# Performance work log

Hardware: AMD Instinct MI355X
Metric: run time of the kernel (lower is better)

Reference implementation:

```python
import jax, jax.numpy as jnp
import numpy as np
import math

HEADS = 16


def setup_inputs() -> dict:
    key = jax.random.key(0)
    kx, kq, kk, kv = jax.random.split(key, 4)
    B, S, E = 2, 2048, 1024
    x = jax.random.normal(kx, (B, S, E), dtype=jnp.float32)
    # torch nn.Linear weights are [out, in]; y = x @ W.T
    Wq = jax.random.normal(kq, (E, E), dtype=jnp.float32) * (1.0 / math.sqrt(E))
    Wk = jax.random.normal(kk, (E, E), dtype=jnp.float32) * (1.0 / math.sqrt(E))
    Wv = jax.random.normal(kv, (E, E), dtype=jnp.float32) * (1.0 / math.sqrt(E))
    # multiplicative causal mask, as the module applies mask by elementwise multiply
    mask = jnp.tril(jnp.ones((S, S), dtype=jnp.float32))
    return {"x": x, "Wq": Wq, "Wk": Wk, "Wv": Wv, "mask": mask}


def reference(x, Wq, Wk, Wv, mask):
    B, S, E = x.shape
    H = HEADS
    D = E // H
    q = (x @ Wq.T).reshape(B, S, H, D)
    k = (x @ Wk.T).reshape(B, S, H, D)
    v = (x @ Wv.T).reshape(B, S, H, D)
    # scores: [B, H, S, S]
    sim = jnp.einsum('nqhd,nkhd->nhqk', q, k)
    sim = sim * mask  # multiplicative mask, broadcast over (B, H)
    # NOTE: original scales by sqrt(emsize), not sqrt(head_dim)
    attn = jax.nn.softmax(sim / math.sqrt(E), axis=-1)
    out = jnp.einsum('nhql,nlhd->nqhd', attn, v).reshape(B, S, E)
    return out
```

## Files before the change

kernel.cpp:

```cpp
#include <hip/hip_runtime.h>
#include <hip/hip_bf16.h>
#include <cstdint>

using bf16   = __bf16;
using bf16x4 = __attribute__((ext_vector_type(4))) __bf16;
using bf16x8 = __attribute__((ext_vector_type(8))) __bf16;
using f32x4  = __attribute__((ext_vector_type(4))) float;

#define MFMA16(a, b, c) __builtin_amdgcn_mfma_f32_16x16x32_bf16((a), (b), (c), 0, 0, 0)

__device__ __forceinline__ void load_lds16(const bf16* g, bf16* l) {
    __builtin_amdgcn_global_load_lds(
        (const __attribute__((address_space(1))) void*)g,
        (__attribute__((address_space(3))) void*)l, 16, 0, 0);
}

__global__ __launch_bounds__(256) void cast_all(const float* __restrict__ x,
                                                const float* __restrict__ Wq,
                                                const float* __restrict__ Wk,
                                                const float* __restrict__ Wv,
                                                bf16* __restrict__ xb,
                                                bf16* __restrict__ wb,
                                                float qscale) {
    int i = blockIdx.x * 256 + threadIdx.x;
    const float* src; bf16* dst; int off; float scale = 1.0f;
    if (i < 1048576)      { src = x;  dst = xb;              off = i; }
    else if (i < 1310720) { src = Wq; dst = wb;              off = i - 1048576; scale = qscale; }
    else if (i < 1572864) { src = Wk; dst = wb + (1u << 20); off = i - 1310720; }
    else                  { src = Wv; dst = wb + (2u << 20); off = i - 1572864; }
    float4 v = reinterpret_cast<const float4*>(src)[off];
    bf16x4 o;
    o[0] = (bf16)(v.x * scale); o[1] = (bf16)(v.y * scale);
    o[2] = (bf16)(v.z * scale); o[3] = (bf16)(v.w * scale);
    reinterpret_cast<bf16x4*>(dst)[off] = o;
}

__global__ __launch_bounds__(256) void qkv_gemm(const bf16* __restrict__ xb,
                                                const bf16* __restrict__ wb,
                                                bf16* __restrict__ Qo,
                                                bf16* __restrict__ Ko,
                                                bf16* __restrict__ Vt) {
    const int n0 = blockIdx.x * 128;
    const int m0 = blockIdx.y * 128;

    __shared__ __align__(16) bf16 As[128 * 64];
    __shared__ __align__(16) bf16 Bs[128 * 64];

    const int t    = threadIdx.x;
    const int lane = t & 63;
    const int wid  = t >> 6;
    const int quad = lane >> 4;
    const int col  = lane & 15;
    const int wm   = wid & 1;
    const int wn   = wid >> 1;

    const int rsub = lane >> 3;
    const int csw  = ((lane & 7) ^ rsub) * 8;

    f32x4 acc[4][4] = {};

    const bf16* Ag = &xb[(size_t)(m0 + rsub) * 1024 + csw];
    const bf16* Bg = &wb[(size_t)(n0 + rsub) * 1024 + csw];

    for (int kc = 0; kc < 1024; kc += 64) {
        __syncthreads();
#pragma unroll
        for (int j = 0; j < 4; ++j) {
            const int c = wid * 4 + j;
            load_lds16(Ag + kc + (size_t)c * 8 * 1024, &As[c * 512]);
        }
#pragma unroll
        for (int j = 0; j < 4; ++j) {
            const int c = wid * 4 + j;
            load_lds16(Bg + kc + (size_t)c * 8 * 1024, &Bs[c * 512]);
        }
        __syncthreads();

#pragma unroll
        for (int ks = 0; ks < 2; ++ks) {
            const int ca = ((ks * 4 + quad) ^ (col & 7)) * 8;
            bf16x8 a[4], b[4];
#pragma unroll
            for (int i = 0; i < 4; ++i)
                a[i] = *reinterpret_cast<const bf16x8*>(
                    &As[(wm * 64 + i * 16 + col) * 64 + ca]);
#pragma unroll
            for (int i = 0; i < 4; ++i)
                b[i] = *reinterpret_cast<const bf16x8*>(
                    &Bs[(wn * 64 + i * 16 + col) * 64 + ca]);
#pragma unroll
            for (int mt = 0; mt < 4; ++mt)
#pragma unroll
                for (int nt = 0; nt < 4; ++nt)
                    acc[mt][nt] = MFMA16(a[mt], b[nt], acc[mt][nt]);
        }
    }

    const int w = blockIdx.x >> 3;
#pragma unroll
    for (int mt = 0; mt < 4; ++mt) {
#pragma unroll
        for (int nt = 0; nt < 4; ++nt) {
#pragma unroll
            for (int r = 0; r < 4; ++r) {
                int m = m0 + wm * 64 + mt * 16 + quad * 4 + r;
                int n = n0 + wn * 64 + nt * 16 + col;
                int bb = m >> 11, s = m & 2047;
                int n1 = n & 1023;
                int h = n1 >> 6, d = n1 & 63;
                size_t bh = (size_t)(bb * 16 + h);
                bf16 v = (bf16)acc[mt][nt][r];
                if (w == 0)      Qo[(bh * 2048 + s) * 64 + d] = v;
                else if (w == 1) Ko[(bh * 2048 + s) * 64 + d] = v;
                else             Vt[(bh * 64 + d) * 2048 + s] = v;
            }
        }
    }
}

__global__ __launch_bounds__(256) void tail_kernel(const bf16* __restrict__ Vt,
                                                   float* __restrict__ Tail) {
    const int bh = blockIdx.x;
    const bf16* Vg = Vt + (size_t)bh * 64 * 2048;
    float* Tg = Tail + (size_t)bh * 33 * 64;

    __shared__ float ts[64 * 33];
    const int tid = threadIdx.x;

#pragma unroll
    for (int i = 0; i < 8; ++i) {
        int task = i * 256 + tid;
        int d = task >> 5, tt = task & 31;
        const bf16* p = &Vg[(size_t)d * 2048 + tt * 64];
        float s = 0.0f;
#pragma unroll
        for (int j = 0; j < 8; ++j) {
            bf16x8 v = *reinterpret_cast<const bf16x8*>(p + j * 8);
#pragma unroll
            for (int e = 0; e < 8; ++e) s += (float)v[e];
        }
        ts[d * 33 + tt] = s;
    }
    __syncthreads();

    if (tid < 64) {
        const int d = tid;
        float s = 0.0f;
        Tg[32 * 64 + d] = 0.0f;
        for (int tt = 31; tt >= 1; --tt) {
            s += ts[d * 33 + tt];
            Tg[tt * 64 + d] = s;
        }
    }
}

__global__ __launch_bounds__(256) void attn_kernel(const bf16* __restrict__ Q,
                                                   const bf16* __restrict__ K,
                                                   const bf16* __restrict__ Vt,
                                                   const float* __restrict__ Tail,
                                                   float* __restrict__ out) {
    const int b = blockIdx.z;
    const int h = blockIdx.y;

    const int t    = threadIdx.x;
    const int lane = t & 63;
    const int wid  = t >> 6;
    const int quad = lane >> 4;
    const int col  = lane & 15;
    const int qh   = wid & 1;
    const int kh   = wid >> 1;

    const int bh = b * 16 + h;
    const bf16* Qg = Q + (size_t)bh * 2048 * 64;
    const bf16* Kg = K + (size_t)bh * 2048 * 64;
    const bf16* Vg = Vt + (size_t)bh * 64 * 2048;

    __shared__ __align__(16) bf16 Ks[128 * 64];
    __shared__ __align__(16) bf16 Vs[64 * 128];
    __shared__ __align__(16) bf16 Ps[64 * 136];

    bf16x8 ones;
#pragma unroll
    for (int i = 0; i < 8; ++i) ones[i] = (bf16)1.0f;

    const int rsubK = lane >> 3;
    const int cswK  = ((lane & 7) ^ rsubK) * 8;
    const int rV    = lane >> 4;
    const int ccV   = lane & 15;

    for (int pp = 0; pp < 2; ++pp) {
        const int qt = pp == 0 ? (31 - (int)blockIdx.x) : (int)blockIdx.x;
        const int q0 = qt * 64;
        const int np = (qt >> 1) + 1;

        bf16x8 qf[2][2];
#pragma unroll
        for (int qs = 0; qs < 2; ++qs)
#pragma unroll
            for (int ks = 0; ks < 2; ++ks)
                qf[qs][ks] = *reinterpret_cast<const bf16x8*>(
                    &Qg[(size_t)(q0 + qh * 32 + qs * 16 + col) * 64 + ks * 32 + quad * 8]);

        f32x4 o[2][2];
        f32x4 la[2];
        {
            const float tc = 64.0f * (float)(32 - 2 * np);
#pragma unroll
            for (int qs = 0; qs < 2; ++qs)
#pragma unroll
                for (int r = 0; r < 4; ++r) la[qs][r] = tc;
            const float* Tg = Tail + ((size_t)bh * 33 + 2 * np) * 64;
#pragma unroll
            for (int dt = 0; dt < 2; ++dt) {
                float tv = Tg[kh * 32 + dt * 16 + col];
#pragma unroll
                for (int qs = 0; qs < 2; ++qs)
#pragma unroll
                    for (int r = 0; r < 4; ++r) o[qs][dt][r] = tv;
            }
        }

        const int s0max = (np - 1) * 128;

        for (int s0 = 0; s0 < np * 128; s0 += 128) {
            __syncthreads();
#pragma unroll
            for (int jj = 0; jj < 4; ++jj) {
                const int c = wid * 4 + jj;
                load_lds16(&Kg[(size_t)(s0 + c * 8 + rsubK) * 64 + cswK], &Ks[c * 512]);
                const int d = c * 4 + rV;
                load_lds16(&Vg[(size_t)d * 2048 + s0 + ((ccV ^ (d & 15)) * 8)], &Vs[c * 512]);
            }
            __syncthreads();

            f32x4 sv[2][4] = {};
            __builtin_amdgcn_s_setprio(1);
#pragma unroll
            for (int ks = 0; ks < 2; ++ks) {
                const int ca = ((ks * 4 + quad) ^ (col & 7)) * 8;
#pragma unroll
                for (int nt = 0; nt < 4; ++nt) {
                    bf16x8 kb = *reinterpret_cast<const bf16x8*>(
                        &Ks[((kh * 4 + nt) * 16 + col) * 64 + ca]);
                    sv[0][nt] = MFMA16(kb, qf[0][ks], sv[0][nt]);
                    sv[1][nt] = MFMA16(kb, qf[1][ks], sv[1][nt]);
                }
            }
            __builtin_amdgcn_s_setprio(0);

            if (s0 == s0max) {
#pragma unroll
                for (int qs = 0; qs < 2; ++qs) {
                    const int qc = q0 + qh * 32 + qs * 16 + col;
#pragma unroll
                    for (int nt = 0; nt < 4; ++nt)
#pragma unroll
                        for (int r = 0; r < 4; ++r) {
                            int kidx = s0 + kh * 64 + nt * 16 + quad * 4 + r;
                            if (kidx > qc) sv[qs][nt][r] = 0.0f;
                        }
                }
            }

#pragma unroll
            for (int qs = 0; qs < 2; ++qs) {
                bf16* Pq = &Ps[(qh * 32 + qs * 16 + col) * 136 + kh * 64];
#pragma unroll
                for (int nt = 0; nt < 4; ++nt) {
                    bf16x4 pw;
#pragma unroll
                    for (int r = 0; r < 4; ++r)
                        pw[r] = (bf16)__builtin_amdgcn_exp2f(sv[qs][nt][r]);
                    *reinterpret_cast<bf16x4*>(&Pq[nt * 16 + quad * 4]) = pw;
                }
            }

            __syncthreads();

            __builtin_amdgcn_s_setprio(1);
#pragma unroll
            for (int kg = 0; kg < 4; ++kg) {
                bf16x8 pa0 = *reinterpret_cast<const bf16x8*>(
                    &Ps[(qh * 32 + col) * 136 + kg * 32 + quad * 8]);
                bf16x8 pa1 = *reinterpret_cast<const bf16x8*>(
                    &Ps[(qh * 32 + 16 + col) * 136 + kg * 32 + quad * 8]);
                la[0] = MFMA16(pa0, ones, la[0]);
                la[1] = MFMA16(pa1, ones, la[1]);
#pragma unroll
                for (int dt = 0; dt < 2; ++dt) {
                    bf16x8 vb = *reinterpret_cast<const bf16x8*>(
                        &Vs[(kh * 32 + dt * 16 + col) * 128 + ((kg * 4 + quad) ^ col) * 8]);
                    o[0][dt] = MFMA16(pa0, vb, o[0][dt]);
                    o[1][dt] = MFMA16(pa1, vb, o[1][dt]);
                }
            }
            __builtin_amdgcn_s_setprio(0);
        }

#pragma unroll
        for (int qs = 0; qs < 2; ++qs) {
#pragma unroll
            for (int r = 0; r < 4; ++r) {
                int q = q0 + qh * 32 + qs * 16 + quad * 4 + r;
                float inv = __builtin_amdgcn_rcpf(la[qs][r]);
#pragma unroll
                for (int dt = 0; dt < 2; ++dt) {
                    int d = kh * 32 + dt * 16 + col;
                    out[((size_t)b * 2048 + q) * 1024 + h * 64 + d] = o[qs][dt][r] * inv;
                }
            }
        }
    }
}

extern "C" void kernel_launch(void* const* d_in, const int* in_sizes, int n_in,
                              void* d_out, int out_size, void* d_ws, size_t ws_size,
                              hipStream_t stream) {
    const float* x  = (const float*)d_in[0];
    const float* Wq = (const float*)d_in[1];
    const float* Wk = (const float*)d_in[2];
    const float* Wv = (const float*)d_in[3];
    float* out = (float*)d_out;

    char* ws = (char*)d_ws;
    bf16*  xb   = (bf16*)(ws);
    bf16*  wb   = (bf16*)(ws + (size_t)(8  << 20));
    bf16*  Qb   = (bf16*)(ws + (size_t)(14 << 20));
    bf16*  Kb   = (bf16*)(ws + (size_t)(22 << 20));
    bf16*  Vtb  = (bf16*)(ws + (size_t)(30 << 20));
    float* Tail = (float*)(ws + (size_t)(38 << 20));

    const float QSCALE = 1.44269504088896f / 32.0f;

    cast_all<<<7168, 256, 0, stream>>>(x, Wq, Wk, Wv, xb, wb, QSCALE);

    qkv_gemm<<<dim3(24, 32), 256, 0, stream>>>(xb, wb, Qb, Kb, Vtb);

    tail_kernel<<<32, 256, 0, stream>>>(Vtb, Tail);

    attn_kernel<<<dim3(16, 16, 2), 256, 0, stream>>>(Qb, Kb, Vtb, Tail, out);
}
```

Baseline: 174.2 us.

## Double-buffer K/V tiles with 64-key steps and remap blocks across XCDs

The attention loop now steps over 64-key tiles instead of 128. The next K and V tiles are loaded into a second LDS buffer while the current tile is computed, which overlaps global loads with MFMA work. Causal masking now skips work at 64-key granularity instead of 128. The grid is flattened to 1D with an XCD-aware block remap, so blocks sharing a (batch, head) tend to run on the same die. In exchange there are more loop iterations and barriers per tile, and the Tail index semantics change to per-64 blocks, which relies on tail_kernel producing 33 entries per 64-key stride.

```diff
diff --git a/kernel.cpp b/kernel.cpp
--- a/kernel.cpp
+++ b/kernel.cpp
@@ -159,8 +159,12 @@
                                                    const bf16* __restrict__ Vt,
                                                    const float* __restrict__ Tail,
                                                    float* __restrict__ out) {
-    const int b = blockIdx.z;
-    const int h = blockIdx.y;
+    const int bid  = blockIdx.x;
+    const int work = (bid & 7) * 64 + (bid >> 3);
+    const int bh   = work >> 4;
+    const int x    = work & 15;
+    const int b    = bh >> 4;
+    const int h    = bh & 15;
 
     const int t    = threadIdx.x;
     const int lane = t & 63;
@@ -170,28 +174,26 @@
     const int qh   = wid & 1;
     const int kh   = wid >> 1;
 
-    const int bh = b * 16 + h;
     const bf16* Qg = Q + (size_t)bh * 2048 * 64;
     const bf16* Kg = K + (size_t)bh * 2048 * 64;
     const bf16* Vg = Vt + (size_t)bh * 64 * 2048;
 
-    __shared__ __align__(16) bf16 Ks[128 * 64];
-    __shared__ __align__(16) bf16 Vs[64 * 128];
-    __shared__ __align__(16) bf16 Ps[64 * 136];
+    __shared__ __align__(16) bf16 Ks[2][64 * 64];
+    __shared__ __align__(16) bf16 Vs[2][64 * 64];
+    __shared__ __align__(16) bf16 Ps[64 * 72];
 
     bf16x8 ones;
 #pragma unroll
     for (int i = 0; i < 8; ++i) ones[i] = (bf16)1.0f;
 
-    const int rsubK = lane >> 3;
-    const int cswK  = ((lane & 7) ^ rsubK) * 8;
-    const int rV    = lane >> 4;
-    const int ccV   = lane & 15;
+    const int r8   = lane >> 3;
+    const int c8   = lane & 7;
+    const int cswK = (c8 ^ r8) * 8;
 
     for (int pp = 0; pp < 2; ++pp) {
-        const int qt = pp == 0 ? (31 - (int)blockIdx.x) : (int)blockIdx.x;
+        const int qt = pp == 0 ? (31 - x) : x;
         const int q0 = qt * 64;
-        const int np = (qt >> 1) + 1;
+        const int nI = qt + 1;
 
         bf16x8 qf[2][2];
 #pragma unroll
@@ -204,12 +206,12 @@
         f32x4 o[2][2];
         f32x4 la[2];
         {
-            const float tc = 64.0f * (float)(32 - 2 * np);
+            const float tc = 64.0f * (float)(32 - nI);
 #pragma unroll
             for (int qs = 0; qs < 2; ++qs)
 #pragma unroll
                 for (int r = 0; r < 4; ++r) la[qs][r] = tc;
-            const float* Tg = Tail + ((size_t)bh * 33 + 2 * np) * 64;
+            const float* Tg = Tail + ((size_t)bh * 33 + nI) * 64;
 #pragma unroll
             for (int dt = 0; dt < 2; ++dt) {
                 float tv = Tg[kh * 32 + dt * 16 + col];
@@ -220,43 +222,53 @@
             }
         }
 
-        const int s0max = (np - 1) * 128;
-
-        for (int s0 = 0; s0 < np * 128; s0 += 128) {
-            __syncthreads();
-#pragma unroll
-            for (int jj = 0; jj < 4; ++jj) {
-                const int c = wid * 4 + jj;
-                load_lds16(&Kg[(size_t)(s0 + c * 8 + rsubK) * 64 + cswK], &Ks[c * 512]);
-                const int d = c * 4 + rV;
-                load_lds16(&Vg[(size_t)d * 2048 + s0 + ((ccV ^ (d & 15)) * 8)], &Vs[c * 512]);
-            }
-            __syncthreads();
-
-            f32x4 sv[2][4] = {};
+#pragma unroll
+        for (int jj = 0; jj < 2; ++jj) {
+            const int w = wid * 2 + jj;
+            load_lds16(&Kg[(size_t)(w * 8 + r8) * 64 + cswK], &Ks[0][w * 512]);
+            load_lds16(&Vg[(size_t)(w * 8 + r8) * 2048 + cswK], &Vs[0][w * 512]);
+        }
+        __syncthreads();
+
+        for (int i = 0; i < nI; ++i) {
+            const int cur  = i & 1;
+            const bool more = (i + 1 < nI);
+            const int s0   = i * 64;
+
+            if (more) {
+                const int s0n = s0 + 64;
+#pragma unroll
+                for (int jj = 0; jj < 2; ++jj) {
+                    const int w = wid * 2 + jj;
+                    load_lds16(&Kg[(size_t)(s0n + w * 8 + r8) * 64 + cswK],
+                               &Ks[cur ^ 1][w * 512]);
+                }
+            }
+
+            f32x4 sv[2][2] = {};
             __builtin_amdgcn_s_setprio(1);
 #pragma unroll
             for (int ks = 0; ks < 2; ++ks) {
                 const int ca = ((ks * 4 + quad) ^ (col & 7)) * 8;
 #pragma unroll
-                for (int nt = 0; nt < 4; ++nt) {
+                for (int nt = 0; nt < 2; ++nt) {
                     bf16x8 kb = *reinterpret_cast<const bf16x8*>(
-                        &Ks[((kh * 4 + nt) * 16 + col) * 64 + ca]);
+                        &Ks[cur][((kh * 2 + nt) * 16 + col) * 64 + ca]);
                     sv[0][nt] = MFMA16(kb, qf[0][ks], sv[0][nt]);
                     sv[1][nt] = MFMA16(kb, qf[1][ks], sv[1][nt]);
                 }
             }
             __builtin_amdgcn_s_setprio(0);
 
-            if (s0 == s0max) {
+            if (i == nI - 1) {
 #pragma unroll
                 for (int qs = 0; qs < 2; ++qs) {
                     const int qc = q0 + qh * 32 + qs * 16 + col;
 #pragma unroll
-                    for (int nt = 0; nt < 4; ++nt)
+                    for (int nt = 0; nt < 2; ++nt)
 #pragma unroll
                         for (int r = 0; r < 4; ++r) {
-                            int kidx = s0 + kh * 64 + nt * 16 + quad * 4 + r;
+                            int kidx = s0 + kh * 32 + nt * 16 + quad * 4 + r;
                             if (kidx > qc) sv[qs][nt][r] = 0.0f;
                         }
                 }
@@ -264,9 +276,9 @@
 
 #pragma unroll
             for (int qs = 0; qs < 2; ++qs) {
-                bf16* Pq = &Ps[(qh * 32 + qs * 16 + col) * 136 + kh * 64];
-#pragma unroll
-                for (int nt = 0; nt < 4; ++nt) {
+                bf16* Pq = &Ps[(qh * 32 + qs * 16 + col) * 72 + kh * 32];
+#pragma unroll
+                for (int nt = 0; nt < 2; ++nt) {
                     bf16x4 pw;
 #pragma unroll
                     for (int r = 0; r < 4; ++r)
@@ -277,24 +289,37 @@
 
             __syncthreads();
 
+            if (more) {
+                const int s0n = s0 + 64;
+#pragma unroll
+                for (int jj = 0; jj < 2; ++jj) {
+                    const int w = wid * 2 + jj;
+                    load_lds16(&Vg[(size_t)(w * 8 + r8) * 2048 + s0n + cswK],
+                               &Vs[cur ^ 1][w * 512]);
+                }
+            }
+
             __builtin_amdgcn_s_setprio(1);
 #pragma unroll
-            for (int kg = 0; kg < 4; ++kg) {
+            for (int kg = 0; kg < 2; ++kg) {
                 bf16x8 pa0 = *reinterpret_cast<const bf16x8*>(
-                    &Ps[(qh * 32 + col) * 136 + kg * 32 + quad * 8]);
+                    &Ps[(qh * 32 + col) * 72 + kg * 32 + quad * 8]);
                 bf16x8 pa1 = *reinterpret_cast<const bf16x8*>(
-                    &Ps[(qh * 32 + 16 + col) * 136 + kg * 32 + quad * 8]);
+                    &Ps[(qh * 32 + 16 + col) * 72 + kg * 32 + quad * 8]);
                 la[0] = MFMA16(pa0, ones, la[0]);
                 la[1] = MFMA16(pa1, ones, la[1]);
 #pragma unroll
                 for (int dt = 0; dt < 2; ++dt) {
                     bf16x8 vb = *reinterpret_cast<const bf16x8*>(
-                        &Vs[(kh * 32 + dt * 16 + col) * 128 + ((kg * 4 + quad) ^ col) * 8]);
+                        &Vs[cur][(kh * 32 + dt * 16 + col) * 64 +
+                                 (((kg * 4 + quad) ^ (col & 7))) * 8]);
                     o[0][dt] = MFMA16(pa0, vb, o[0][dt]);
                     o[1][dt] = MFMA16(pa1, vb, o[1][dt]);
                 }
             }
             __builtin_amdgcn_s_setprio(0);
+
+            __syncthreads();
         }
 
 #pragma unroll
@@ -338,5 +363,5 @@
 
     tail_kernel<<<32, 256, 0, stream>>>(Vtb, Tail);
 
-    attn_kernel<<<dim3(16, 16, 2), 256, 0, stream>>>(Qb, Kb, Vtb, Tail, out);
-}
+    attn_kernel<<<512, 256, 0, stream>>>(Qb, Kb, Vtb, Tail, out);
+}
```

Measured after the change: 177.9 us. 2.1% more time.
